# Kernel tuning notes

Hardware: AMD Instinct MI355X
Metric: run time of the kernel (lower is better)

## Reference

```python
import jax, jax.numpy as jnp
import numpy as np

B, C_ENC, H, W = 8, 512, 96, 96
N_SAMP = 64            # num_samples in forward
N_NODES = 2 * N_SAMP   # 64 pos + 64 neg per image
D = 256                # node feature dim after head_in_ln
N_HEADS = 8
DH = D // N_HEADS
SINKHORN_ITERS = 10


def _ln(x):
    # LayerNorm(elementwise_affine=False)
    m = x.mean(-1, keepdims=True)
    v = x.var(-1, keepdims=True)
    return (x - m) / jnp.sqrt(v + 1e-5)


def setup_inputs() -> dict:
    key = jax.random.key(0)
    ks = jax.random.split(key, 12)
    std = 0.01  # matches nn.init.normal_(std=0.01) in _init_weights
    inp = {
        "feat_s": jax.random.normal(ks[0], (B, C_ENC, H, W), jnp.float32),
        "score_s": jax.random.normal(ks[1], (B, 1, H, W), jnp.float32),
        "feat_t": jax.random.normal(ks[2], (B, C_ENC, H, W), jnp.float32),
        "score_t": jax.random.normal(ks[3], (B, 1, H, W), jnp.float32),
        "head_W1": std * jax.random.normal(ks[4], (C_ENC, D), jnp.float32),
        "head_b1": jnp.zeros((D,), jnp.float32),
        "head_W2": std * jax.random.normal(ks[5], (D, D), jnp.float32),
        "head_b2": jnp.zeros((D,), jnp.float32),
        "intra_W": jax.random.normal(ks[6], (4, D, D), jnp.float32) / jnp.sqrt(jnp.float32(D)),
        "intra_b": jnp.zeros((4, D), jnp.float32),
        "cross_W": jax.random.normal(ks[7], (4, D, D), jnp.float32) / jnp.sqrt(jnp.float32(D)),
        "cross_b": jnp.zeros((4, D), jnp.float32),
        "cls_W1": std * jax.random.normal(ks[8], (D, 128), jnp.float32),
        "cls_b1": jnp.zeros((128,), jnp.float32),
        "cls_W2": std * jax.random.normal(ks[9], (128, 1), jnp.float32),
        "cls_b2": jnp.zeros((1,), jnp.float32),
        "aff_A": jax.random.normal(ks[10], (D, D), jnp.float32) / jnp.sqrt(jnp.float32(D)),
    }
    return inp


def _sample_points(feat, score):
    # torch version: boolean-mask nonzero + random gather of 64 pos / 64 neg spatial
    # locations per image. JIT-friendly deterministic equivalent: top-64 highest
    # sigmoid scores = positives, top-64 lowest = negatives.
    s = jax.nn.sigmoid(score[:, 0].reshape(B, -1))            # [B, H*W]
    _, pos_idx = jax.lax.top_k(s, N_SAMP)
    _, neg_idx = jax.lax.top_k(-s, N_SAMP)
    idx = jnp.concatenate([pos_idx, neg_idx], axis=1)         # [B, 128]
    ff = feat.reshape(B, C_ENC, -1)                           # [B, 512, H*W]
    nodes = jnp.take_along_axis(ff, idx[:, None, :], axis=2)  # [B, 512, 128]
    nodes = nodes.transpose(0, 2, 1)                          # [B, 128, 512]
    labels = jnp.concatenate(
        [jnp.ones((B, N_SAMP, 1), feat.dtype), jnp.zeros((B, N_SAMP, 1), feat.dtype)], axis=1)
    return nodes, labels


def _mha(xq, xkv, Wp, bp):
    # standard multi-head attention (MultiHeadAttentionWrapper)
    q = xq @ Wp[0] + bp[0]
    k = xkv @ Wp[1] + bp[1]
    v = xkv @ Wp[2] + bp[2]
    sh = lambda t: t.reshape(t.shape[0], t.shape[1], N_HEADS, DH)
    att = jnp.einsum("bqhd,bkhd->bhqk", sh(q), sh(k)) / jnp.sqrt(jnp.float32(DH))
    att = jax.nn.softmax(att, axis=-1)
    o = jnp.einsum("bhqk,bkhd->bqhd", att, sh(v)).reshape(xq.shape[0], xq.shape[1], D)
    return o @ Wp[3] + bp[3], att.mean(1)


def _forward(feat_s, score_s, feat_t, score_t, head_W1, head_b1, head_W2, head_b2,
             intra_W, intra_b, cross_W, cross_b, cls_W1, cls_b1, cls_W2, cls_b2, aff_A):
    n1, l1 = _sample_points(feat_s, score_s)
    n2, l2 = _sample_points(feat_t, score_t)

    # head_in_ln: Linear -> LN -> ReLU -> Linear -> LN
    head = lambda x: _ln(jax.nn.relu(_ln(x @ head_W1 + head_b1)) @ head_W2 + head_b2)
    n1, n2 = head(n1), head(n2)

    # intra-domain graph (self-attention), shared weights for both domains
    n1, _ = _mha(n1, n1, intra_W, intra_b)
    n2, _ = _mha(n2, n2, intra_W, intra_b)

    # cross-domain graph (cross-attention both directions, shared weights)
    c1, _ = _mha(n1, n2, cross_W, cross_b)
    c2, _ = _mha(n2, n1, cross_W, cross_b)
    n1, n2 = c1, c2

    # node classification loss (BCEWithLogits, mean)
    cls = lambda x: jax.nn.relu(x @ cls_W1 + cls_b1) @ cls_W2 + cls_b2
    def bce_logits(logit, lab):
        return jnp.mean(jnp.maximum(logit, 0) - logit * lab + jnp.log1p(jnp.exp(-jnp.abs(logit))))
    node_loss = bce_logits(cls(n1), l1) + bce_logits(cls(n2), l2)

    # affinity + InstanceNorm2d(1) + sinkhorn refine
    Mmat = jnp.einsum("bnd,de,bme->bnm", n1, aff_A, n2)       # [B, 128, 128]
    mu = Mmat.mean((1, 2), keepdims=True)
    var = Mmat.var((1, 2), keepdims=True)
    K = (Mmat - mu) / jnp.sqrt(var + 1e-5)
    for _ in range(SINKHORN_ITERS):  # log-space row/col normalization
        K = K - jax.nn.logsumexp(K, axis=2, keepdims=True)
        K = K - jax.nn.logsumexp(K, axis=1, keepdims=True)
    P = jnp.exp(K)

    # matching loss = BCEFocalLoss(gamma=2, alpha=0.25) vs label-agreement matrix
    gt = (l1[:, :, 0][:, :, None] == l2[:, :, 0][:, None, :]).astype(P.dtype)
    pt = jnp.clip(P, 1e-6, 1.0 - 1e-6)
    mat_loss = jnp.mean(-0.25 * (1 - pt) ** 2 * gt * jnp.log(pt)
                        - 0.75 * pt ** 2 * (1 - gt) * jnp.log(1 - pt))

    total_loss = node_loss + 10.0 * mat_loss
    return n1, total_loss


def reference(feat_s, score_s, feat_t, score_t, head_W1, head_b1, head_W2, head_b2,
              intra_W, intra_b, cross_W, cross_b, cls_W1, cls_b1, cls_W2, cls_b2, aff_A):
    return _forward(feat_s, score_s, feat_t, score_t, head_W1, head_b1, head_W2, head_b2,
                    intra_W, intra_b, cross_W, cross_b, cls_W1, cls_b1, cls_W2, cls_b2, aff_A)
```

## Files before the change

### kernel.cpp

```cpp
#include <hip/hip_runtime.h>
#include <math.h>

#define BIMG 8
#define HW 9216
#define CENC 512
#define NN 128
#define DD 256
#define NHEAD 8
#define DH 32
#define ROWS1 1024
#define ROWS2 2048
#define TAILB 520

typedef unsigned long long ull;
typedef unsigned short u16;
typedef __attribute__((ext_vector_type(4))) float f32x4;
typedef __attribute__((ext_vector_type(4))) unsigned u32x4;
typedef __attribute__((ext_vector_type(2))) unsigned u32x2;

__device__ __forceinline__ u16 f2bf(float f) {
  unsigned u = __float_as_uint(f);
  u += 0x7fffu + ((u >> 16) & 1u);
  return (u16)(u >> 16);
}
__device__ __forceinline__ float bf2f(unsigned h) { return __uint_as_float(h << 16); }
__device__ __forceinline__ unsigned pack2(float a, float b) {
  return (unsigned)f2bf(a) | ((unsigned)f2bf(b) << 16);
}
__device__ __forceinline__ void mfma_b(f32x4& acc, u32x4 a, u32x4 b) {
  asm volatile("v_mfma_f32_16x16x32_bf16 %0, %1, %2, %0" : "+v"(acc) : "v"(a), "v"(b));
}
__device__ __forceinline__ void mfma_s(f32x4& acc, u32x4 a, u32x4 b) {
  asm volatile("s_nop 1\n\tv_mfma_f32_16x16x32_bf16 %0, %1, %2, %0" : "+v"(acc) : "v"(a), "v"(b));
}

__device__ __forceinline__ ull cmpex_keep(ull k, ull o, bool keepMax) {
  return ((k > o) == keepMax) ? k : o;
}
__device__ __forceinline__ void bsort64(ull& k, int lane) {
#pragma unroll
  for (int size = 2; size <= 64; size <<= 1) {
#pragma unroll
    for (int stride = size >> 1; stride > 0; stride >>= 1) {
      ull o = __shfl_xor(k, stride);
      bool keepMax = (((lane & size) == 0) == ((lane & stride) == 0));
      k = cmpex_keep(k, o, keepMax);
    }
  }
}
__device__ __forceinline__ void bmerge64(ull& top, ull b, int lane) {
  ull rev = __shfl_xor(b, 63);
  ull m = top > rev ? top : rev;
#pragma unroll
  for (int stride = 32; stride > 0; stride >>= 1) {
    ull o = __shfl_xor(m, stride);
    m = cmpex_keep(m, o, (lane & stride) == 0);
  }
  top = m;
}
__device__ __forceinline__ ull lds_merge(ull a, ull brev, int lane) {
  ull m = a > brev ? a : brev;
#pragma unroll
  for (int stride = 32; stride > 0; stride >>= 1) {
    ull o = __shfl_xor(m, stride);
    m = cmpex_keep(m, o, (lane & stride) == 0);
  }
  return m;
}

__global__ __launch_bounds__(512) void head_kernel(const float* __restrict__ score_s,
                                                   const float* __restrict__ score_t,
                                                   int* __restrict__ idx_out,
                                                   float* __restrict__ loss_acc,
                                                   const float* __restrict__ hw1,
                                                   const float* __restrict__ hw2,
                                                   const float* __restrict__ iw,
                                                   const float* __restrict__ cw,
                                                   const float* __restrict__ aw,
                                                   const float* __restrict__ clsW1,
                                                   const float* __restrict__ intra_b,
                                                   const float* __restrict__ cross_b,
                                                   u16* __restrict__ wt,
                                                   u16* __restrict__ w1t,
                                                   u16* __restrict__ wt_f,
                                                   float* __restrict__ bfq) {
  __shared__ union {
    struct { ull sm[512]; float tile[32][33]; } a;
    struct { float Wo[32][264]; float Wc[256][40]; } b;
  } HS;
  int tid = threadIdx.x;
  if (blockIdx.x < 32) {
    int blk = blockIdx.x;
    int bi = blk >> 1, neg = blk & 1;
    int lane = tid & 63, w = tid >> 6;
    if (blk == 0 && tid < 4) loss_acc[tid] = 0.f;
    const float* sp = (bi < 8 ? score_s : score_t) + (size_t)(bi & 7) * HW;
    int q0 = w * 18;
    ull keys[18];
#pragma unroll
    for (int j = 0; j < 18; ++j) {
      float x = sp[(q0 + j) * 64 + lane];
      unsigned ub = __float_as_uint(x);
      unsigned u = (ub & 0x80000000u) ? ~ub : (ub | 0x80000000u);
      if (neg) u = ~u;
      int gi = (q0 + j) * 64 + lane;
      keys[j] = ((ull)u << 32) | (unsigned)(~gi);
    }
    ull top1 = keys[0]; bsort64(top1, lane);
    ull top2 = keys[9]; bsort64(top2, lane);
#pragma unroll
    for (int j = 1; j < 9; ++j) {
      ull k1 = keys[j], k2 = keys[9 + j];
      bsort64(k1, lane);
      bsort64(k2, lane);
      bmerge64(top1, k1, lane);
      bmerge64(top2, k2, lane);
    }
    bmerge64(top1, top2, lane);
    HS.a.sm[w * 64 + lane] = top1;
    __syncthreads();
    if (w < 4) {
      ull m = lds_merge(HS.a.sm[(2 * w) * 64 + lane],
                        HS.a.sm[(2 * w + 1) * 64 + (63 - lane)], lane);
      HS.a.sm[(2 * w) * 64 + lane] = m;
    }
    __syncthreads();
    if (w < 2) {
      ull m = lds_merge(HS.a.sm[(4 * w) * 64 + lane],
                        HS.a.sm[(4 * w + 2) * 64 + (63 - lane)], lane);
      HS.a.sm[(4 * w) * 64 + lane] = m;
    }
    __syncthreads();
    if (w == 0) {
      ull m = lds_merge(HS.a.sm[lane], HS.a.sm[4 * 64 + (63 - lane)], lane);
      idx_out[bi * NN + neg * 64 + lane] = (int)(~(unsigned)(m & 0xffffffffull));
    }
  } else if (blockIdx.x < 800) {
    int bid = blockIdx.x - 32;
    const float* src; u16* dst; int K, k0, n0;
    if (bid < 128) {
      src = hw1; dst = wt; K = 512;
      k0 = (bid >> 3) * 32; n0 = (bid & 7) * 32;
    } else {
      int id2 = bid - 128;
      int m = id2 >> 6, tt = id2 & 63;
      K = 256;
      k0 = (tt >> 3) * 32; n0 = (tt & 7) * 32;
      src = (m == 0) ? hw2 : (m < 5) ? iw + (size_t)(m - 1) * 65536
          : (m < 9) ? cw + (size_t)(m - 5) * 65536 : aw;
      dst = wt + 131072 + (size_t)m * 65536;
    }
    int r = tid >> 3, c = (tid & 7) * 4;
    if (tid < 256) {
      float4 v = *(const float4*)&src[(size_t)(k0 + r) * 256 + n0 + c];
      HS.a.tile[r][c] = v.x; HS.a.tile[r][c + 1] = v.y;
      HS.a.tile[r][c + 2] = v.z; HS.a.tile[r][c + 3] = v.w;
    }
    __syncthreads();
    if (tid < 256) {
      u32x2 o;
      o[0] = pack2(HS.a.tile[c][r], HS.a.tile[c + 1][r]);
      o[1] = pack2(HS.a.tile[c + 2][r], HS.a.tile[c + 3][r]);
      *(u32x2*)&dst[(size_t)(n0 + r) * K + k0 + c] = o;
    }
  } else if (blockIdx.x < 832) {
    int bid3 = blockIdx.x - 800;
    int k0 = (bid3 >> 2) * 32, n0 = (bid3 & 3) * 32;
    int r = tid >> 3, c = (tid & 7) * 4;
    if (tid < 256) {
      float4 v = *(const float4*)&clsW1[(size_t)(k0 + r) * 128 + n0 + c];
      HS.a.tile[r][c] = v.x; HS.a.tile[r][c + 1] = v.y;
      HS.a.tile[r][c + 2] = v.z; HS.a.tile[r][c + 3] = v.w;
    }
    __syncthreads();
    if (tid < 256) {
      u32x2 o;
      o[0] = pack2(HS.a.tile[c][r], HS.a.tile[c + 1][r]);
      o[1] = pack2(HS.a.tile[c + 2][r], HS.a.tile[c + 3][r]);
      *(u32x2*)&w1t[(size_t)(n0 + r) * 256 + k0 + c] = o;
    }
  } else {
    int bid4 = blockIdx.x - 832;
    int z = bid4 >> 6, tt = bid4 & 63;
    int k0 = (tt >> 3) * 32, n0 = (tt & 7) * 32;
    const float* Wo = iw + 3 * 65536;
    const float* Wc = cw + (size_t)z * 65536;
    for (int e = tid; e < 2048; e += 512) {
      int row = e >> 6, c4 = (e & 63) * 4;
      *(float4*)&HS.b.Wo[row][c4] = *(const float4*)&Wo[(size_t)(k0 + row) * 256 + c4];
    }
    for (int e = tid; e < 2048; e += 512) {
      int row = e >> 3, c4 = (e & 7) * 4;
      *(float4*)&HS.b.Wc[row][c4] = *(const float4*)&Wc[(size_t)row * 256 + n0 + c4];
    }
    __syncthreads();
    int k = tid >> 4, half = (tid >> 3) & 1, nb = (tid & 7) * 4;
    float a0 = 0.f, a1 = 0.f, a2 = 0.f, a3 = 0.f;
    int jb = half * 128;
#pragma unroll 8
    for (int j = 0; j < 128; ++j) {
      float wo = HS.b.Wo[k][jb + j];
      float4 wc = *(const float4*)&HS.b.Wc[jb + j][nb];
      a0 += wo * wc.x; a1 += wo * wc.y; a2 += wo * wc.z; a3 += wo * wc.w;
    }
    a0 += __shfl_xor(a0, 8); a1 += __shfl_xor(a1, 8);
    a2 += __shfl_xor(a2, 8); a3 += __shfl_xor(a3, 8);
    if (half == 0) {
      u16* dst = wt_f + (size_t)z * 65536;
      dst[(size_t)(n0 + nb + 0) * 256 + k0 + k] = f2bf(a0);
      dst[(size_t)(n0 + nb + 1) * 256 + k0 + k] = f2bf(a1);
      dst[(size_t)(n0 + nb + 2) * 256 + k0 + k] = f2bf(a2);
      dst[(size_t)(n0 + nb + 3) * 256 + k0 + k] = f2bf(a3);
    }
    if (k0 == 0 && tid < 32) {
      float b = 0.f;
      const float* bo = intra_b + 768;
      for (int j = 0; j < 256; ++j) b += bo[j] * HS.b.Wc[j][tid];
      bfq[z * 256 + n0 + tid] = b + cross_b[z * 256 + n0 + tid];
    }
  }
}

__global__ __launch_bounds__(512) void gemm12_fused(const float* __restrict__ feat_s,
                                                    const float* __restrict__ feat_t,
                                                    const int* __restrict__ idxb,
                                                    const u16* __restrict__ wt_h1,
                                                    const float* __restrict__ head_b1,
                                                    const u16* __restrict__ wt_h2,
                                                    const float* __restrict__ head_b2,
                                                    u16* __restrict__ bufB,
                                                    float* __restrict__ st2) {
  __shared__ u16 As[16][520];
  __shared__ u16 Yb[16][264];
  __shared__ u16 Bs[256][40];
  __shared__ float sums[16][16], sqs[16][16], mS[16], rS[16];
  int t = threadIdx.x, l = t & 63, w = t >> 6;
  int m0 = blockIdx.x * 16;
#pragma unroll
  for (int row = 0; row < 16; ++row) {
    int grow = m0 + row;
    int bi = grow >> 7, n = grow & 127, b = bi & 7;
    const float* fp = (bi < 8) ? feat_s : feat_t;
    int pos = idxb[bi * NN + n];
    As[row][t] = f2bf(fp[(size_t)b * CENC * HW + (size_t)t * HW + pos]);
  }
  __syncthreads();
  f32x4 acc[2];
  acc[0] = (f32x4){0.f, 0.f, 0.f, 0.f};
  acc[1] = (f32x4){0.f, 0.f, 0.f, 0.f};
  for (int kc = 0; kc < 16; ++kc) {
#pragma unroll
    for (int i = 0; i < 2; ++i) {
      int e = t + i * 512;
      int nn2 = e >> 2, ch8 = (e & 3) * 8;
      *(u32x4*)&Bs[nn2][ch8] = *(const u32x4*)&wt_h1[(size_t)nn2 * 512 + kc * 32 + ch8];
    }
    __syncthreads();
    u32x4 af = *(const u32x4*)&As[l & 15][kc * 32 + (l >> 4) * 8];
#pragma unroll
    for (int i = 0; i < 2; ++i) {
      u32x4 bf = *(const u32x4*)&Bs[w * 32 + i * 16 + (l & 15)][(l >> 4) * 8];
      mfma_b(acc[i], af, bf);
    }
    __syncthreads();
  }
  asm volatile("s_nop 7\n\ts_nop 7" ::);
#pragma unroll
  for (int i = 0; i < 2; ++i) {
    int col = w * 32 + i * 16 + (l & 15);
    float bb = head_b1[col];
#pragma unroll
    for (int r = 0; r < 4; ++r) {
      int row = (l >> 4) * 4 + r;
      float o = acc[i][r] + bb;
      Yb[row][col] = f2bf(o);
      float s = o, q = o * o;
#pragma unroll
      for (int m = 1; m < 16; m <<= 1) { s += __shfl_xor(s, m); q += __shfl_xor(q, m); }
      if ((l & 15) == 0) {
        sums[row][w * 2 + i] = s;
        sqs[row][w * 2 + i]  = q;
      }
    }
  }
  __syncthreads();
  if (t < 16) {
    float s = 0.f, q = 0.f;
#pragma unroll
    for (int i = 0; i < 16; ++i) { s += sums[t][i]; q += sqs[t][i]; }
    float mm = s * (1.f / 256.f);
    mS[t] = mm;
    rS[t] = rsqrtf(fmaxf(q * (1.f / 256.f) - mm * mm, 0.f) + 1e-5f);
  }
  __syncthreads();
  {
    int row = t >> 5, c8 = (t & 31) * 8;
    u32x4 v = *(const u32x4*)&Yb[row][c8];
    float mm = mS[row], rr = rS[row];
#pragma unroll
    for (int j = 0; j < 4; ++j) {
      float f0 = fmaxf((bf2f(v[j] & 0xffffu) - mm) * rr, 0.f);
      float f1 = fmaxf((bf2f(v[j] >> 16) - mm) * rr, 0.f);
      v[j] = pack2(f0, f1);
    }
    __syncthreads();
    *(u32x4*)&Yb[row][c8] = v;
  }
  __syncthreads();
#pragma unroll
  for (int i = 0; i < 2; ++i) {
    int n0 = (w * 2 + i) * 16;
    f32x4 a2 = {0.f, 0.f, 0.f, 0.f};
    int ar = l & 15;
    int bn = n0 + (l & 15);
#pragma unroll
    for (int ks = 0; ks < 8; ++ks) {
      int ak = ks * 32 + (l >> 4) * 8;
      u32x4 af = *(const u32x4*)&Yb[ar][ak];
      u32x4 bf = *(const u32x4*)&wt_h2[(size_t)bn * 256 + ak];
      mfma_b(a2, af, bf);
    }
    asm volatile("s_nop 7\n\ts_nop 7" ::);
    float bb = head_b2[n0 + (l & 15)];
#pragma unroll
    for (int r = 0; r < 4; ++r) {
      int row = m0 + (l >> 4) * 4 + r;
      float o = a2[r] + bb;
      bufB[(size_t)row * 256 + n0 + (l & 15)] = f2bf(o);
      float s = o, q = o * o;
#pragma unroll
      for (int m = 1; m < 16; m <<= 1) { s += __shfl_xor(s, m); q += __shfl_xor(q, m); }
      if ((l & 15) == 0) {
        st2[(size_t)row * 32 + w * 2 + i]      = s;
        st2[(size_t)row * 32 + 16 + w * 2 + i] = q;
      }
    }
  }
}

template<int K>
__global__ __launch_bounds__(512) void gemm_mf(const u16* __restrict__ A,
                                               const u16* __restrict__ Wt,
                                               const float* __restrict__ bias,
                                               u16* __restrict__ Cb,
                                               float* __restrict__ Cf,
                                               int ldc,
                                               const float* __restrict__ in_stats, int in_relu,
                                               float* __restrict__ out_stats) {
  constexpr int LDK = K + 8;
  constexpr int KC = K / 8;
  __shared__ u16 As[32][LDK];
  __shared__ u16 Bs[64][LDK];
  __shared__ float mS[32], rS[32];
  int n0 = blockIdx.x * 64, m0 = blockIdx.y * 32;
  int t = threadIdx.x;
  if (in_stats) {
    if (t < 32) {
      const float* sp = in_stats + (size_t)(m0 + t) * 32;
      float s = 0.f, q = 0.f;
#pragma unroll
      for (int i = 0; i < 16; ++i) { s += sp[i]; q += sp[16 + i]; }
      float mm = s * (1.f / 256.f);
      float var = q * (1.f / 256.f) - mm * mm;
      mS[t] = mm;
      rS[t] = rsqrtf(fmaxf(var, 0.f) + 1e-5f);
    }
    __syncthreads();
  }
  for (int i = t; i < 32 * KC; i += 512) {
    int row = i / KC, c8 = (i % KC) * 8;
    u32x4 av = *(const u32x4*)&A[(size_t)(m0 + row) * K + c8];
    if (in_stats) {
      float mm = mS[row], rr = rS[row];
#pragma unroll
      for (int j = 0; j < 4; ++j) {
        float f0 = (bf2f(av[j] & 0xffffu) - mm) * rr;
        float f1 = (bf2f(av[j] >> 16) - mm) * rr;
        if (in_relu) { f0 = fmaxf(f0, 0.f); f1 = fmaxf(f1, 0.f); }
        av[j] = pack2(f0, f1);
      }
    }
    *(u32x4*)&As[row][c8] = av;
  }
  for (int i = t; i < 64 * KC; i += 512) {
    int row = i / KC, c8 = (i % KC) * 8;
    *(u32x4*)&Bs[row][c8] = *(const u32x4*)&Wt[(size_t)(n0 + row) * K + c8];
  }
  __syncthreads();
  int l = t & 63, w = t >> 6;
  int wr = w >> 2, wc = w & 3;
  int fra = wr * 16 + (l & 15);
  int frk = (l >> 4) * 8;
  int fb = wc * 16 + (l & 15);
  f32x4 acc = {0.f, 0.f, 0.f, 0.f};
#pragma unroll
  for (int ks = 0; ks < K / 32; ++ks) {
    u32x4 af = *(const u32x4*)&As[fra][ks * 32 + frk];
    u32x4 bf = *(const u32x4*)&Bs[fb][ks * 32 + frk];
    mfma_b(acc, af, bf);
  }
  asm volatile("s_nop 7\n\ts_nop 7" ::);
  int col0 = n0 + wc * 16 + (l & 15);
  int rbase = m0 + wr * 16 + (l >> 4) * 4;
  float b0 = bias ? bias[col0] : 0.f;
#pragma unroll
  for (int r = 0; r < 4; ++r) {
    int row = rbase + r;
    float o0 = acc[r] + b0;
    if (Cb) Cb[(size_t)row * 256 + col0] = f2bf(o0);
    if (Cf && row < ROWS1) Cf[(size_t)row * ldc + col0] = o0;
    if (out_stats) {
      float s0 = o0, q0 = o0 * o0;
#pragma unroll
      for (int m = 1; m < 16; m <<= 1) { s0 += __shfl_xor(s0, m); q0 += __shfl_xor(q0, m); }
      if ((l & 15) == 0) {
        int slot = (n0 >> 4) + wc;
        out_stats[(size_t)row * 32 + slot]      = s0;
        out_stats[(size_t)row * 32 + 16 + slot] = q0;
      }
    }
  }
}

template<int HASLN, int SWAP>
__global__ __launch_bounds__(1024) void fattn_kernel(const u16* __restrict__ X,
                                                     const u16* __restrict__ Wt,
                                                     const float* __restrict__ bias,
                                                     const float* __restrict__ stats,
                                                     u16* __restrict__ O) {
  __shared__ u16 Qs[128][40];
  __shared__ u16 Ks[128][40];
  __shared__ u16 Vt[32][136];
  __shared__ float Sf[128][132];
  __shared__ u16 Pb[128][136];
  __shared__ float mS[128], rS[128], dn[128];
  int blk = blockIdx.x;
  int bb = blk >> 3, h = blk & 7;
  int kb = SWAP ? (bb ^ 8) : bb;
  int baseQ = bb * 128, baseKV = kb * 128;
  int t = threadIdx.x, l = t & 63, w = t >> 6;
  if (HASLN) {
    if (t < 128) {
      const float* sp = stats + (size_t)(baseQ + t) * 32;
      float s = 0.f, q = 0.f;
#pragma unroll
      for (int i = 0; i < 16; ++i) { s += sp[i]; q += sp[16 + i]; }
      float mm = s * (1.f / 256.f);
      mS[t] = mm;
      rS[t] = rsqrtf(fmaxf(q * (1.f / 256.f) - mm * mm, 0.f) + 1e-5f);
    }
    __syncthreads();
  }
  const float scale = 0.17677669529663687f;
  int mt = w >> 1, nt = w & 1;
#pragma unroll
  for (int z = 0; z < 3; ++z) {
    const u16* Xz = X + (size_t)(z == 0 ? baseQ : baseKV) * 256;
    f32x4 acc = {0.f, 0.f, 0.f, 0.f};
    int ar = mt * 16 + (l & 15);
    int bn = h * 32 + nt * 16 + (l & 15);
#pragma unroll
    for (int ks = 0; ks < 8; ++ks) {
      int ak = ks * 32 + (l >> 4) * 8;
      u32x4 af = *(const u32x4*)&Xz[(size_t)ar * 256 + ak];
      if (HASLN) {
        float mm = mS[ar], rr = rS[ar];
#pragma unroll
        for (int j = 0; j < 4; ++j) {
          float f0 = (bf2f(af[j] & 0xffffu) - mm) * rr;
          float f1 = (bf2f(af[j] >> 16) - mm) * rr;
          af[j] = pack2(f0, f1);
        }
      }
      u32x4 bf = *(const u32x4*)&Wt[(size_t)z * 65536 + (size_t)bn * 256 + ak];
      mfma_s(acc, af, bf);
    }
    asm volatile("s_nop 7\n\ts_nop 7" ::);
    float bv = bias[z * 256 + h * 32 + nt * 16 + (l & 15)];
    int cn = nt * 16 + (l & 15);
#pragma unroll
    for (int r2 = 0; r2 < 4; ++r2) {
      int rr2 = mt * 16 + (l >> 4) * 4 + r2;
      float v = acc[r2] + bv;
      if (z == 0)      Qs[rr2][cn] = f2bf(v);
      else if (z == 1) Ks[rr2][cn] = f2bf(v);
      else             Vt[cn][rr2] = f2bf(v);
    }
  }
  __syncthreads();
#pragma unroll
  for (int i = 0; i < 4; ++i) {
    int tile = w * 4 + i, mt2 = tile >> 3, nt2 = tile & 7;
    f32x4 acc = {0.f, 0.f, 0.f, 0.f};
    u32x4 af = *(const u32x4*)&Qs[mt2 * 16 + (l & 15)][(l >> 4) * 8];
    u32x4 bf = *(const u32x4*)&Ks[nt2 * 16 + (l & 15)][(l >> 4) * 8];
    mfma_s(acc, af, bf);
    asm volatile("s_nop 7\n\ts_nop 7" ::);
#pragma unroll
    for (int r2 = 0; r2 < 4; ++r2)
      Sf[mt2 * 16 + (l >> 4) * 4 + r2][nt2 * 16 + (l & 15)] = acc[r2] * scale;
  }
  __syncthreads();
  {
    int r = t >> 3, p = t & 7;
    int js = p * 16;
    float v[16];
#pragma unroll
    for (int q4 = 0; q4 < 4; ++q4) {
      float4 f = *(const float4*)&Sf[r][js + q4 * 4];
      v[q4 * 4 + 0] = f.x; v[q4 * 4 + 1] = f.y; v[q4 * 4 + 2] = f.z; v[q4 * 4 + 3] = f.w;
    }
    float mx = v[0];
#pragma unroll
    for (int j = 1; j < 16; ++j) mx = fmaxf(mx, v[j]);
    for (int m = 1; m < 8; m <<= 1) mx = fmaxf(mx, __shfl_xor(mx, m));
    float e[16];
    float den = 0.f;
#pragma unroll
    for (int j = 0; j < 16; ++j) { e[j] = __expf(v[j] - mx); den += e[j]; }
    for (int m = 1; m < 8; m <<= 1) den += __shfl_xor(den, m);
    unsigned* pw = (unsigned*)&Pb[r][js];
#pragma unroll
    for (int jp = 0; jp < 8; ++jp) pw[jp] = pack2(e[2 * jp], e[2 * jp + 1]);
    if (p == 0) dn[r] = 1.0f / den;
  }
  __syncthreads();
  {
    f32x4 acc = {0.f, 0.f, 0.f, 0.f};
#pragma unroll
    for (int ks = 0; ks < 4; ++ks) {
      u32x4 af = *(const u32x4*)&Pb[mt * 16 + (l & 15)][ks * 32 + (l >> 4) * 8];
      u32x4 bf = *(const u32x4*)&Vt[nt * 16 + (l & 15)][ks * 32 + (l >> 4) * 8];
      mfma_s(acc, af, bf);
    }
    asm volatile("s_nop 7\n\ts_nop 7" ::);
    int cn = nt * 16 + (l & 15);
#pragma unroll
    for (int r2 = 0; r2 < 4; ++r2) {
      int rr2 = mt * 16 + (l >> 4) * 4 + r2;
      O[(size_t)(baseQ + rr2) * 256 + h * 32 + cn] = f2bf(acc[r2] * dn[rr2]);
    }
  }
}

struct SkSmem {
  union { u16 tmpL[128][264]; float Km[128][133]; } u;
  float u_[NN];
  float v_[NN];
  float red[20];
};
struct ClsSmem {
  float xs[4][256];
  float part[4][128];
  float red[8];
};
union TailSmem { SkSmem sk; ClsSmem cls; };

__device__ __forceinline__ void ticket_finalize(float* acc, float* out) {
  __threadfence();
  int tk = atomicAdd((int*)acc + 3, 1);
  if (tk == TAILB - 1) {
    float a0 = atomicAdd(acc + 0, 0.0f);
    float a1 = atomicAdd(acc + 1, 0.0f);
    out[ROWS1 * DD] = a0 + 10.0f * a1;
  }
}

__global__ __launch_bounds__(1024) void tail_kernel(const u16* __restrict__ bufH,
                                                    const u16* __restrict__ wt_af,
                                                    const u16* __restrict__ w1t,
                                                    const float* __restrict__ b1,
                                                    const float* __restrict__ W2,
                                                    const float* __restrict__ b2,
                                                    float* __restrict__ acc,
                                                    float* __restrict__ out) {
  __shared__ TailSmem sm;
  int t = threadIdx.x;
  int bid = blockIdx.x;
  if (bid < 8) {
    int b = bid;
    int l = t & 63, w = t >> 6;
    int tr = w >> 1;
    const u16* c1 = bufH + (size_t)(b * 128) * 256;
    const u16* c2 = bufH + (size_t)(1024 + b * 128) * 256;
    {
      int tcB = (w & 1) * 8;
      f32x4 accA[8];
#pragma unroll
      for (int i = 0; i < 8; ++i) accA[i] = (f32x4){0.f, 0.f, 0.f, 0.f};
      for (int ks = 0; ks < 8; ++ks) {
        int kk = ks * 32 + (l >> 4) * 8;
        u32x4 af = *(const u32x4*)&c1[(size_t)(tr * 16 + (l & 15)) * 256 + kk];
#pragma unroll
        for (int i = 0; i < 8; ++i) {
          u32x4 bf = *(const u32x4*)&wt_af[(size_t)((tcB + i) * 16 + (l & 15)) * 256 + kk];
          mfma_b(accA[i], af, bf);
        }
      }
      asm volatile("s_nop 7\n\ts_nop 7" ::);
      int rb = tr * 16 + (l >> 4) * 4;
#pragma unroll
      for (int i = 0; i < 8; ++i) {
        int col = (tcB + i) * 16 + (l & 15);
#pragma unroll
        for (int r2 = 0; r2 < 4; ++r2)
          sm.sk.u.tmpL[rb + r2][col] = f2bf(accA[i][r2]);
      }
    }
    __syncthreads();
    f32x4 aB[4];
    {
      int tcB = (w & 1) * 4;
#pragma unroll
      for (int i = 0; i < 4; ++i) aB[i] = (f32x4){0.f, 0.f, 0.f, 0.f};
      for (int ks = 0; ks < 8; ++ks) {
        int kk = ks * 32 + (l >> 4) * 8;
        u32x4 a0 = *(const u32x4*)&sm.sk.u.tmpL[tr * 16 + (l & 15)][kk];
#pragma unroll
        for (int i = 0; i < 4; ++i) {
          u32x4 bf = *(const u32x4*)&c2[(size_t)((tcB + i) * 16 + (l & 15)) * 256 + kk];
          mfma_b(aB[i], a0, bf);
        }
      }
      asm volatile("s_nop 7\n\ts_nop 7" ::);
    }
    __syncthreads();
    {
      int tcB = (w & 1) * 4;
      int rb = tr * 16 + (l >> 4) * 4;
#pragma unroll
      for (int i = 0; i < 4; ++i) {
        int col = (tcB + i) * 16 + (l & 15);
#pragma unroll
        for (int r2 = 0; r2 < 4; ++r2)
          sm.sk.u.Km[rb + r2][col] = aB[i][r2];
      }
    }
    __syncthreads();
    int r = t >> 3, cg = t & 7;
    int c = t >> 3, rg = t & 7;
    float kr[16], kc[16];
    {
#pragma unroll
      for (int q4 = 0; q4 < 4; ++q4) {
        float4 f = *(const float4*)&sm.sk.u.Km[r][cg * 16 + q4 * 4];
        kr[q4 * 4 + 0] = f.x; kr[q4 * 4 + 1] = f.y; kr[q4 * 4 + 2] = f.z; kr[q4 * 4 + 3] = f.w;
      }
#pragma unroll
      for (int q = 0; q < 16; ++q)
        kc[q] = sm.sk.u.Km[rg * 16 + q][c];
    }
    float s = 0.f;
#pragma unroll
    for (int q = 0; q < 16; ++q) s += kr[q];
    for (int m = 1; m < 64; m <<= 1) s += __shfl_xor(s, m);
    if ((t & 63) == 0) sm.sk.red[t >> 6] = s;
    __syncthreads();
    if (t == 0) { float tt = 0.f; for (int i = 0; i < 16; ++i) tt += sm.sk.red[i]; sm.sk.red[16] = tt; }
    __syncthreads();
    float mu = sm.sk.red[16] * (1.0f / 16384.f);
    __syncthreads();
    float sq = 0.f;
#pragma unroll
    for (int q = 0; q < 16; ++q) { float d = kr[q] - mu; sq += d * d; }
    for (int m = 1; m < 64; m <<= 1) sq += __shfl_xor(sq, m);
    if ((t & 63) == 0) sm.sk.red[t >> 6] = sq;
    __syncthreads();
    if (t == 0) { float tt = 0.f; for (int i = 0; i < 16; ++i) tt += sm.sk.red[i]; sm.sk.red[17] = tt; }
    __syncthreads();
    float inv = 1.0f / sqrtf(sm.sk.red[17] * (1.0f / 16384.f) + 1e-5f);
#pragma unroll
    for (int q = 0; q < 16; ++q) { kr[q] = (kr[q] - mu) * inv; kc[q] = (kc[q] - mu) * inv; }
    if (t < NN) { sm.sk.u_[t] = 0.f; sm.sk.v_[t] = 0.f; }
    __syncthreads();
    for (int iter = 0; iter < 10; ++iter) {
      float tmp[16];
      {
        const float4* vp = (const float4*)(sm.sk.v_ + cg * 16);
#pragma unroll
        for (int q4 = 0; q4 < 4; ++q4) {
          float4 f = vp[q4];
          tmp[q4 * 4 + 0] = kr[q4 * 4 + 0] - f.x; tmp[q4 * 4 + 1] = kr[q4 * 4 + 1] - f.y;
          tmp[q4 * 4 + 2] = kr[q4 * 4 + 2] - f.z; tmp[q4 * 4 + 3] = kr[q4 * 4 + 3] - f.w;
        }
        float mx = tmp[0];
#pragma unroll
        for (int q = 1; q < 16; ++q) mx = fmaxf(mx, tmp[q]);
        for (int m = 1; m < 8; m <<= 1) mx = fmaxf(mx, __shfl_xor(mx, m));
        float smv = 0.f;
#pragma unroll
        for (int q = 0; q < 16; ++q) smv += __expf(tmp[q] - mx);
        for (int m = 1; m < 8; m <<= 1) smv += __shfl_xor(smv, m);
        if (cg == 0) sm.sk.u_[r] = mx + __logf(smv);
      }
      __syncthreads();
      {
        const float4* up = (const float4*)(sm.sk.u_ + rg * 16);
#pragma unroll
        for (int q4 = 0; q4 < 4; ++q4) {
          float4 f = up[q4];
          tmp[q4 * 4 + 0] = kc[q4 * 4 + 0] - f.x; tmp[q4 * 4 + 1] = kc[q4 * 4 + 1] - f.y;
          tmp[q4 * 4 + 2] = kc[q4 * 4 + 2] - f.z; tmp[q4 * 4 + 3] = kc[q4 * 4 + 3] - f.w;
        }
        float mx = tmp[0];
#pragma unroll
        for (int q = 1; q < 16; ++q) mx = fmaxf(mx, tmp[q]);
        for (int m = 1; m < 8; m <<= 1) mx = fmaxf(mx, __shfl_xor(mx, m));
        float smv = 0.f;
#pragma unroll
        for (int q = 0; q < 16; ++q) smv += __expf(tmp[q] - mx);
        for (int m = 1; m < 8; m <<= 1) smv += __shfl_xor(smv, m);
        if (rg == 0) sm.sk.v_[c] = mx + __logf(smv);
      }
      __syncthreads();
    }
    float ur = sm.sk.u_[r];
    float fsum = 0.f;
    {
      const float4* vp = (const float4*)(sm.sk.v_ + cg * 16);
#pragma unroll
      for (int q4 = 0; q4 < 4; ++q4) {
        float4 f = vp[q4];
        float vv[4] = {f.x, f.y, f.z, f.w};
#pragma unroll
        for (int j = 0; j < 4; ++j) {
          float P = __expf(kr[q4 * 4 + j] - ur - vv[j]);
          float pt = fminf(fmaxf(P, 1e-6f), 1.0f - 1e-6f);
          int col = cg * 16 + q4 * 4 + j;
          bool gt = (r < 64) == (col < 64);
          float wgt = gt ? (-0.25f * (1.f - pt) * (1.f - pt)) : (-0.75f * pt * pt);
          float lg = gt ? __logf(pt) : __logf(1.f - pt);
          fsum += wgt * lg;
        }
      }
    }
    for (int m = 1; m < 64; m <<= 1) fsum += __shfl_xor(fsum, m);
    if ((t & 63) == 0) sm.sk.red[t >> 6] = fsum;
    __syncthreads();
    if (t == 0) {
      float tt = 0.f; for (int i = 0; i < 16; ++i) tt += sm.sk.red[i];
      atomicAdd(acc + 1, tt * (1.0f / 131072.f));
      ticket_finalize(acc, out);
    }
  } else {
    int row0 = (bid - 8) * 4;
    {
      int rr = t >> 8, cc = t & 255;
      sm.cls.xs[rr][cc] = bf2f(bufH[(size_t)(row0 + rr) * 256 + cc]);
    }
    __syncthreads();
    int grp = t >> 8, col = t & 127, kh = (t >> 7) & 1;
    const u16* wp = w1t + (size_t)col * 256 + kh * 128;
    const float* xp = &sm.cls.xs[grp][kh * 128];
    float h = 0.f;
#pragma unroll
    for (int i = 0; i < 16; ++i) {
      u32x4 wv = *(const u32x4*)&wp[i * 8];
      const float* x8 = xp + i * 8;
      h += x8[0] * bf2f(wv[0] & 0xffffu) + x8[1] * bf2f(wv[0] >> 16)
         + x8[2] * bf2f(wv[1] & 0xffffu) + x8[3] * bf2f(wv[1] >> 16)
         + x8[4] * bf2f(wv[2] & 0xffffu) + x8[5] * bf2f(wv[2] >> 16)
         + x8[6] * bf2f(wv[3] & 0xffffu) + x8[7] * bf2f(wv[3] >> 16);
    }
    if (kh == 1) sm.cls.part[grp][col] = h;
    __syncthreads();
    if (kh == 0) {
      float z = h + sm.cls.part[grp][col] + b1[col];
      float p = fmaxf(z, 0.f) * W2[col];
#pragma unroll
      for (int m = 1; m < 64; m <<= 1) p += __shfl_xor(p, m);
      if ((t & 63) == 0) sm.cls.red[grp * 2 + ((t >> 6) & 1)] = p;
    }
    __syncthreads();
    if (t == 0) {
      float total = 0.f;
      float bb2 = b2[0];
#pragma unroll
      for (int g = 0; g < 4; ++g) {
        float z = sm.cls.red[2 * g] + sm.cls.red[2 * g + 1] + bb2;
        float lab = (((row0 + g) & 127) < 64) ? 1.f : 0.f;
        total += fmaxf(z, 0.f) - z * lab + log1pf(__expf(-fabsf(z)));
      }
      atomicAdd(acc, total * (1.0f / 1024.0f));
      ticket_finalize(acc, out);
    }
  }
}

extern "C" void kernel_launch(void* const* d_in, const int* in_sizes, int n_in,
                              void* d_out, int out_size, void* d_ws, size_t ws_size,
                              hipStream_t stream) {
  const float* feat_s  = (const float*)d_in[0];
  const float* score_s = (const float*)d_in[1];
  const float* feat_t  = (const float*)d_in[2];
  const float* score_t = (const float*)d_in[3];
  const float* head_W1 = (const float*)d_in[4];
  const float* head_b1 = (const float*)d_in[5];
  const float* head_W2 = (const float*)d_in[6];
  const float* head_b2 = (const float*)d_in[7];
  const float* intra_W = (const float*)d_in[8];
  const float* intra_b = (const float*)d_in[9];
  const float* cross_W = (const float*)d_in[10];
  const float* cross_b = (const float*)d_in[11];
  const float* cls_W1  = (const float*)d_in[12];
  const float* cls_b1  = (const float*)d_in[13];
  const float* cls_W2  = (const float*)d_in[14];
  const float* cls_b2  = (const float*)d_in[15];
  const float* aff_A   = (const float*)d_in[16];

  u16* bufB  = (u16*)d_ws;
  u16* bufH  = bufB + ROWS2 * DD;
  u16* attnb = bufH + ROWS2 * DD;
  u16* atto2 = attnb + ROWS2 * DD;
  u16* wt    = atto2 + ROWS2 * DD;
  u16* w1t   = wt + 786432;
  u16* wt_f  = w1t + 32768;
  float* st2 = (float*)(wt_f + 3 * 65536);
  float* bfq = st2 + ROWS2 * 32;
  float* acc = bfq + 768;
  int* idxb  = (int*)(acc + 8);
  float* out_f = (float*)d_out;

  u16* wt_h1 = wt;
  u16* wt_h2 = wt + 131072;
  u16* wt_in = wt_h2 + 65536;
  u16* wt_cr = wt_in + 4 * 65536;
  u16* wt_af = wt_cr + 4 * 65536;

  head_kernel<<<1024, 512, 0, stream>>>(score_s, score_t, idxb, acc,
                                        head_W1, head_W2, intra_W, cross_W, aff_A, cls_W1,
                                        intra_b, cross_b, wt, w1t, wt_f, bfq);
  gemm12_fused<<<128, 512, 0, stream>>>(feat_s, feat_t, idxb, wt_h1, head_b1,
                                        wt_h2, head_b2, bufB, st2);

  dim3 g1(4, 64, 1);
  const float* nulf = nullptr;
  float* nulw = nullptr;

  fattn_kernel<1, 0><<<128, 1024, 0, stream>>>(bufB, wt_in, intra_b, st2, attnb);
  fattn_kernel<0, 1><<<128, 1024, 0, stream>>>(attnb, wt_f, bfq, nulf, atto2);
  gemm_mf<256><<<g1, 512, 0, stream>>>(atto2, wt_cr + 3 * 65536, cross_b + 768, bufH, out_f,
                                       256, nulf, 0, nulw);
  tail_kernel<<<TAILB, 1024, 0, stream>>>(bufH, wt_af, w1t, cls_b1, cls_W2, cls_b2,
                                          acc, out_f);
}
```

Measured before the change: 207.8 us.

## Split attention query rows across two blocks to double grid parallelism

The fused attention kernel now launches 256 blocks of 512 threads instead of 128 blocks of 1024. Each block handles 64 query rows of one image and head. The Q projection is restricted to those rows, while each block still recomputes the full 128-row K and V projections. The aim is to fill more compute units on the chip, at the cost of computing the K/V projection twice per image and head.

```diff
diff --git a/kernel.cpp b/kernel.cpp
--- a/kernel.cpp
+++ b/kernel.cpp
@@ -423,25 +423,25 @@
 }
 
 template<int HASLN, int SWAP>
-__global__ __launch_bounds__(1024) void fattn_kernel(const u16* __restrict__ X,
-                                                     const u16* __restrict__ Wt,
-                                                     const float* __restrict__ bias,
-                                                     const float* __restrict__ stats,
-                                                     u16* __restrict__ O) {
-  __shared__ u16 Qs[128][40];
+__global__ __launch_bounds__(512) void fattn_kernel(const u16* __restrict__ X,
+                                                    const u16* __restrict__ Wt,
+                                                    const float* __restrict__ bias,
+                                                    const float* __restrict__ stats,
+                                                    u16* __restrict__ O) {
+  __shared__ u16 Qs[64][40];
   __shared__ u16 Ks[128][40];
   __shared__ u16 Vt[32][136];
-  __shared__ float Sf[128][132];
-  __shared__ u16 Pb[128][136];
-  __shared__ float mS[128], rS[128], dn[128];
+  __shared__ float Sf[64][132];
+  __shared__ u16 Pb[64][136];
+  __shared__ float mS[128], rS[128], dn[64];
   int blk = blockIdx.x;
-  int bb = blk >> 3, h = blk & 7;
+  int bb = blk >> 4, h = (blk >> 1) & 7, qh = blk & 1;
   int kb = SWAP ? (bb ^ 8) : bb;
-  int baseQ = bb * 128, baseKV = kb * 128;
+  int baseQ = bb * 128 + qh * 64, baseKV = kb * 128;
   int t = threadIdx.x, l = t & 63, w = t >> 6;
   if (HASLN) {
     if (t < 128) {
-      const float* sp = stats + (size_t)(baseQ + t) * 32;
+      const float* sp = stats + (size_t)(kb * 128 + t) * 32;
       float s = 0.f, q = 0.f;
 #pragma unroll
       for (int i = 0; i < 16; ++i) { s += sp[i]; q += sp[16 + i]; }
@@ -453,18 +453,16 @@
   }
   const float scale = 0.17677669529663687f;
   int mt = w >> 1, nt = w & 1;
-#pragma unroll
-  for (int z = 0; z < 3; ++z) {
-    const u16* Xz = X + (size_t)(z == 0 ? baseQ : baseKV) * 256;
+  {
     f32x4 acc = {0.f, 0.f, 0.f, 0.f};
     int ar = mt * 16 + (l & 15);
     int bn = h * 32 + nt * 16 + (l & 15);
 #pragma unroll
     for (int ks = 0; ks < 8; ++ks) {
       int ak = ks * 32 + (l >> 4) * 8;
-      u32x4 af = *(const u32x4*)&Xz[(size_t)ar * 256 + ak];
+      u32x4 af = *(const u32x4*)&X[(size_t)(baseQ + ar) * 256 + ak];
       if (HASLN) {
-        float mm = mS[ar], rr = rS[ar];
+        float mm = mS[qh * 64 + ar], rr = rS[qh * 64 + ar];
 #pragma unroll
         for (int j = 0; j < 4; ++j) {
           float f0 = (bf2f(af[j] & 0xffffu) - mm) * rr;
@@ -472,19 +470,49 @@
           af[j] = pack2(f0, f1);
         }
       }
-      u32x4 bf = *(const u32x4*)&Wt[(size_t)z * 65536 + (size_t)bn * 256 + ak];
+      u32x4 bf = *(const u32x4*)&Wt[(size_t)bn * 256 + ak];
       mfma_s(acc, af, bf);
     }
     asm volatile("s_nop 7\n\ts_nop 7" ::);
-    float bv = bias[z * 256 + h * 32 + nt * 16 + (l & 15)];
+    float bv = bias[h * 32 + nt * 16 + (l & 15)];
     int cn = nt * 16 + (l & 15);
 #pragma unroll
-    for (int r2 = 0; r2 < 4; ++r2) {
-      int rr2 = mt * 16 + (l >> 4) * 4 + r2;
-      float v = acc[r2] + bv;
-      if (z == 0)      Qs[rr2][cn] = f2bf(v);
-      else if (z == 1) Ks[rr2][cn] = f2bf(v);
-      else             Vt[cn][rr2] = f2bf(v);
+    for (int r2 = 0; r2 < 4; ++r2)
+      Qs[mt * 16 + (l >> 4) * 4 + r2][cn] = f2bf(acc[r2] + bv);
+  }
+#pragma unroll
+  for (int z = 1; z < 3; ++z) {
+#pragma unroll
+    for (int kv = 0; kv < 2; ++kv) {
+      f32x4 acc = {0.f, 0.f, 0.f, 0.f};
+      int ar = mt * 16 + (l & 15);
+      int bn = h * 32 + nt * 16 + (l & 15);
+#pragma unroll
+      for (int ks = 0; ks < 8; ++ks) {
+        int ak = ks * 32 + (l >> 4) * 8;
+        u32x4 af = *(const u32x4*)&X[(size_t)(baseKV + kv * 64 + ar) * 256 + ak];
+        if (HASLN) {
+          float mm = mS[kv * 64 + ar], rr = rS[kv * 64 + ar];
+#pragma unroll
+          for (int j = 0; j < 4; ++j) {
+            float f0 = (bf2f(af[j] & 0xffffu) - mm) * rr;
+            float f1 = (bf2f(af[j] >> 16) - mm) * rr;
+            af[j] = pack2(f0, f1);
+          }
+        }
+        u32x4 bf = *(const u32x4*)&Wt[(size_t)z * 65536 + (size_t)bn * 256 + ak];
+        mfma_s(acc, af, bf);
+      }
+      asm volatile("s_nop 7\n\ts_nop 7" ::);
+      float bv = bias[z * 256 + h * 32 + nt * 16 + (l & 15)];
+      int cn = nt * 16 + (l & 15);
+#pragma unroll
+      for (int r2 = 0; r2 < 4; ++r2) {
+        int rr2 = kv * 64 + mt * 16 + (l >> 4) * 4 + r2;
+        float v = acc[r2] + bv;
+        if (z == 1) Ks[rr2][cn] = f2bf(v);
+        else        Vt[cn][rr2] = f2bf(v);
+      }
     }
   }
   __syncthreads();
@@ -837,8 +865,8 @@
   const float* nulf = nullptr;
   float* nulw = nullptr;
 
-  fattn_kernel<1, 0><<<128, 1024, 0, stream>>>(bufB, wt_in, intra_b, st2, attnb);
-  fattn_kernel<0, 1><<<128, 1024, 0, stream>>>(attnb, wt_f, bfq, nulf, atto2);
+  fattn_kernel<1, 0><<<256, 512, 0, stream>>>(bufB, wt_in, intra_b, st2, attnb);
+  fattn_kernel<0, 1><<<256, 512, 0, stream>>>(attnb, wt_f, bfq, nulf, atto2);
   gemm_mf<256><<<g1, 512, 0, stream>>>(atto2, wt_cr + 3 * 65536, cross_b + 768, bufH, out_f,
                                        256, nulf, 0, nulw);
   tail_kernel<<<TAILB, 1024, 0, stream>>>(bufH, wt_af, w1t, cls_b1, cls_W2, cls_b2,
```

After: 195.7 us. -5.8%, faster.
